# Optimization experiments

Hardware: AMD Instinct MI355X
Metric: run time of the kernel (lower is better)

The kernel has to match this reference:

```python
import jax, jax.numpy as jnp
import numpy as np

N_NODES = 40000
N_EDGES = 640000
N_GRAPHS = 64
D_IN = 128
HID = 200
OUT = 2


def _lin(key, fin, fout):
    # torch nn.Linear-style init: U(-1/sqrt(fin), 1/sqrt(fin))
    kw, kb = jax.random.split(key)
    s = 1.0 / np.sqrt(fin)
    W = jax.random.uniform(kw, (fin, fout), jnp.float32, -s, s)
    b = jax.random.uniform(kb, (fout,), jnp.float32, -s, s)
    return W, b


def setup_inputs() -> dict:
    key = jax.random.key(0)
    ks = jax.random.split(key, 10)
    x = jax.random.normal(ks[0], (N_NODES, D_IN), jnp.float32)
    edge_index = jax.random.randint(ks[1], (2, N_EDGES), 0, N_NODES, jnp.int32)
    batch = jnp.sort(jax.random.randint(ks[2], (N_NODES,), 0, N_GRAPHS, jnp.int32))
    W1, b1 = _lin(ks[3], D_IN, HID)
    W2, b2 = _lin(ks[4], HID, HID)
    W3, b3 = _lin(ks[5], HID, HID)
    Wg, bg = _lin(ks[6], HID, HID)
    Wc1, bc1 = _lin(ks[7], HID, HID // 2)
    Wc2, bc2 = _lin(ks[8], HID // 2, OUT)
    return {"x": x, "edge_index": edge_index, "batch": batch,
            "W1": W1, "b1": b1, "W2": W2, "b2": b2, "W3": W3, "b3": b3,
            "Wg": Wg, "bg": bg, "Wc1": Wc1, "bc1": bc1, "Wc2": Wc2, "bc2": bc2}


def reference(x, edge_index, batch, W1, b1, W2, b2, W3, b3, Wg, bg, Wc1, bc1, Wc2, bc2):
    n = x.shape[0]
    # GCNConv with self-loops + symmetric normalization (PyG defaults)
    loop = jnp.arange(n, dtype=edge_index.dtype)
    src = jnp.concatenate([edge_index[0], loop])  # [E+N]
    dst = jnp.concatenate([edge_index[1], loop])
    deg = jax.ops.segment_sum(jnp.ones(src.shape, x.dtype), dst, num_segments=n)
    dinv = jax.lax.rsqrt(jnp.maximum(deg, 1.0))  # deg >= 1 with self-loops
    norm = (dinv[src] * dinv[dst])[:, None]      # [E+N, 1]

    def gcn(h, W, b):
        m = (h @ W)[src] * norm                  # gather + scale per edge
        return jax.ops.segment_sum(m, dst, num_segments=n) + b

    h = jax.nn.relu(gcn(x, W1, b1))
    h = jax.nn.relu(gcn(h, W2, b2))
    h = jax.nn.relu(gcn(h, W3, b3))

    gate = jax.nn.sigmoid(h @ Wg + bg)
    hg = h * gate

    # global_mean_pool over batch assignment
    sums = jax.ops.segment_sum(hg, batch, num_segments=N_GRAPHS)
    cnt = jax.ops.segment_sum(jnp.ones((n,), x.dtype), batch, num_segments=N_GRAPHS)
    pooled = sums / jnp.maximum(cnt, 1.0)[:, None]

    # classifier (dropout is identity in eval)
    hidden = jax.nn.relu(pooled @ Wc1 + bc1)
    logits = hidden @ Wc2 + bc2                  # [N_GRAPHS, 2]
    return logits
```

## Files before the change

### kernel.cpp

```cpp
#include <hip/hip_runtime.h>

#define NG 64
#define HIDW 200
#define DIN 128
#define KPAD 224
#define POOL_NC 8

typedef _Float16 half4_t __attribute__((ext_vector_type(4)));
typedef _Float16 half8_t __attribute__((ext_vector_type(8)));
typedef float floatx4 __attribute__((ext_vector_type(4)));


__global__ void build_kernel(const int* __restrict__ dst, int* __restrict__ counts,
                             const int* __restrict__ batch, int* __restrict__ gs,
                             int E, int n) {
  int i = blockIdx.x * 256 + threadIdx.x;
  if (i < E) atomicAdd(&counts[dst[i]], 1);
  if (i < n) {
    int b = batch[i];
    if (i == 0) {
      for (int g = 0; g <= b; ++g) gs[g] = 0;
    } else {
      int bp = batch[i - 1];
      for (int g = bp + 1; g <= b; ++g) gs[g] = i;
    }
    if (i == n - 1) {
      for (int g = b + 1; g <= NG; ++g) gs[g] = n;
    }
  }
}


__global__ __launch_bounds__(256) void scan1_kernel(const int* __restrict__ counts,
                                                    int* __restrict__ blocksum,
                                                    float* __restrict__ dinv, int n) {
  __shared__ int s[256];
  int tid = threadIdx.x;
  int i = blockIdx.x * 256 + tid;
  int c = (i < n) ? counts[i] : 0;
  if (i < n) dinv[i] = rsqrtf((float)(c + 1));
  s[tid] = c;
  __syncthreads();
#pragma unroll
  for (int off = 128; off > 0; off >>= 1) {
    if (tid < off) s[tid] += s[tid + off];
    __syncthreads();
  }
  if (tid == 0) blocksum[blockIdx.x] = s[0];
}

__global__ __launch_bounds__(1024) void scan2_kernel(int* __restrict__ blocksum, int nb) {
  __shared__ int s[1024];
  int tid = threadIdx.x;
  int v = (tid < nb) ? blocksum[tid] : 0;
  s[tid] = v;
  __syncthreads();
  for (int off = 1; off < 1024; off <<= 1) {
    int t = (tid >= off) ? s[tid - off] : 0;
    __syncthreads();
    s[tid] += t;
    __syncthreads();
  }
  if (tid < nb) blocksum[tid] = s[tid] - v;
}

__global__ __launch_bounds__(256) void scan3_kernel(const int* __restrict__ counts,
                                                    const int* __restrict__ blocksum,
                                                    int* __restrict__ row_ptr, int n) {
  __shared__ int s[256];
  int tid = threadIdx.x;
  int i = blockIdx.x * 256 + tid;
  int c = (i < n) ? counts[i] : 0;
  s[tid] = c;
  __syncthreads();
  for (int off = 1; off < 256; off <<= 1) {
    int t = (tid >= off) ? s[tid - off] : 0;
    __syncthreads();
    s[tid] += t;
    __syncthreads();
  }
  int base = blocksum[blockIdx.x];
  if (i < n) row_ptr[i] = base + s[tid] - c;
  if (i == n - 1) row_ptr[n] = base + s[tid];
}

__global__ void fill_kernel(const int* __restrict__ src, const int* __restrict__ dst,
                            const int* __restrict__ row_ptr, int* __restrict__ fill,
                            int* __restrict__ csr_src, int E) {
  int e = blockIdx.x * 256 + threadIdx.x;
  if (e >= E) return;
  int d = dst[e];
  int pos = row_ptr[d] + atomicAdd(&fill[d], 1);
  csr_src[pos] = src[e];
}


__global__ void wprep_kernel(const float* __restrict__ W1, const float* __restrict__ W2,
                             const float* __restrict__ W3, const float* __restrict__ Wg,
                             _Float16* __restrict__ o1h, _Float16* __restrict__ o1l,
                             _Float16* __restrict__ o2h, _Float16* __restrict__ o2l,
                             _Float16* __restrict__ o3h, _Float16* __restrict__ o3l,
                             _Float16* __restrict__ ogh, _Float16* __restrict__ ogl) {
  int wsel = blockIdx.y;
  const float* W = (wsel == 0) ? W1 : (wsel == 1) ? W2 : (wsel == 2) ? W3 : Wg;
  _Float16* WTh = (wsel == 0) ? o1h : (wsel == 1) ? o2h : (wsel == 2) ? o3h : ogh;
  _Float16* WTl = (wsel == 0) ? o1l : (wsel == 1) ? o2l : (wsel == 2) ? o3l : ogl;
  int K  = (wsel == 0) ? DIN : HIDW;
  int KP = (wsel == 0) ? DIN : KPAD;
  int idx = blockIdx.x * 256 + threadIdx.x;
  if (idx >= 256 * KP) return;
  int col = idx / KP, k = idx % KP;
  float v = (col < HIDW && k < K) ? W[(long)k * HIDW + col] : 0.f;
  _Float16 h = (_Float16)v;
  WTh[idx] = h;
  WTl[idx] = (_Float16)(v - (float)h);
}


__global__ void cvt_kernel(const float* __restrict__ x, const float* __restrict__ dinv,
                           _Float16* __restrict__ g0, int n) {
  int t = blockIdx.x * 256 + threadIdx.x;
  if (t >= n * 32) return;
  int node = t >> 5, q = t & 31;
  float di = dinv[node];
  float4 v = *(const float4*)&x[(long)node * 128 + q * 4];
  half4_t r = {(_Float16)(di * v.x), (_Float16)(di * v.y),
               (_Float16)(di * v.z), (_Float16)(di * v.w)};
  ((half4_t*)g0)[(long)node * 32 + q] = r;
}


template <int C>
__global__ __launch_bounds__(256) void agg_kernel(const _Float16* __restrict__ g,
                                                  const int* __restrict__ row_ptr,
                                                  const int* __restrict__ csr_src,
                                                  const float* __restrict__ dinv,
                                                  _Float16* __restrict__ out, int n) {
  int node = blockIdx.x * 4 + (threadIdx.x >> 6);
  int lane = threadIdx.x & 63;
  if (node >= n || lane >= C) return;
  const half4_t* __restrict__ hp = (const half4_t*)g;
  int e0 = row_ptr[node], e1 = row_ptr[node + 1];
  half4_t self = hp[(long)node * C + lane];
  float ax = (float)self.x, ay = (float)self.y;
  float az = (float)self.z, aw = (float)self.w;

  int e = e0;
  for (; e + 16 <= e1; e += 16) {
    int sI[16];
#pragma unroll
    for (int j = 0; j < 16; ++j) sI[j] = csr_src[e + j];
    half4_t vv[16];
#pragma unroll
    for (int j = 0; j < 16; ++j) vv[j] = hp[(long)sI[j] * C + lane];
#pragma unroll
    for (int j = 0; j < 16; ++j) {
      ax += (float)vv[j].x; ay += (float)vv[j].y;
      az += (float)vv[j].z; aw += (float)vv[j].w;
    }
  }
  if (e + 8 <= e1) {
    int sI[8];
#pragma unroll
    for (int j = 0; j < 8; ++j) sI[j] = csr_src[e + j];
    half4_t vv[8];
#pragma unroll
    for (int j = 0; j < 8; ++j) vv[j] = hp[(long)sI[j] * C + lane];
#pragma unroll
    for (int j = 0; j < 8; ++j) {
      ax += (float)vv[j].x; ay += (float)vv[j].y;
      az += (float)vv[j].z; aw += (float)vv[j].w;
    }
    e += 8;
  }
  if (e + 4 <= e1) {
    int sI[4];
#pragma unroll
    for (int j = 0; j < 4; ++j) sI[j] = csr_src[e + j];
    half4_t vv[4];
#pragma unroll
    for (int j = 0; j < 4; ++j) vv[j] = hp[(long)sI[j] * C + lane];
#pragma unroll
    for (int j = 0; j < 4; ++j) {
      ax += (float)vv[j].x; ay += (float)vv[j].y;
      az += (float)vv[j].z; aw += (float)vv[j].w;
    }
    e += 4;
  }
  for (; e < e1; ++e) {
    int s = csr_src[e];
    half4_t v = hp[(long)s * C + lane];
    ax += (float)v.x; ay += (float)v.y; az += (float)v.z; aw += (float)v.w;
  }
  float di = dinv[node];
  half4_t r = {(_Float16)(di * ax), (_Float16)(di * ay),
               (_Float16)(di * az), (_Float16)(di * aw)};
  ((half4_t*)out)[(long)node * C + lane] = r;
}


template <int KP, int MODE, int DSCALE>
__global__ __launch_bounds__(256, 2) void mgemm_kernel(const _Float16* __restrict__ A,
                                                       const _Float16* __restrict__ WTh,
                                                       const _Float16* __restrict__ WTl,
                                                       const float* __restrict__ bias,
                                                       const float* __restrict__ dinv,
                                                       _Float16* __restrict__ out, int N) {
  constexpr int LDK = KP + 8;
  __shared__ _Float16 Bh[64][LDK];
  __shared__ _Float16 Bl[64][LDK];
  int tid = threadIdx.x;
  int strip = blockIdx.x & 3;
  int rg = blockIdx.x >> 2;
  int col0 = strip * 64;

  {
    int c = tid >> 2;
    int ks = (tid & 3) * (KP / 4);
    const _Float16* gh = WTh + (long)(col0 + c) * KP + ks;
    const _Float16* gl = WTl + (long)(col0 + c) * KP + ks;
#pragma unroll
    for (int j = 0; j < KP / 32; ++j) {
      *(half8_t*)&Bh[c][ks + j * 8] = *(const half8_t*)(gh + j * 8);
      *(half8_t*)&Bl[c][ks + j * 8] = *(const half8_t*)(gl + j * 8);
    }
  }
  __syncthreads();

  int lane = tid & 63;
  int wid = tid >> 6;
  int row0 = rg * 256 + wid * 64;
  if (row0 >= N) return;
  int l15 = lane & 15;
  int lq = lane >> 4;

  const _Float16* __restrict__ pa = A + (long)(row0 + l15) * KP + lq * 8;

  floatx4 acc[4][4];
#pragma unroll
  for (int i = 0; i < 4; ++i)
#pragma unroll
    for (int j = 0; j < 4; ++j) acc[i][j] = (floatx4){0.f, 0.f, 0.f, 0.f};

#pragma unroll
  for (int k0 = 0; k0 < KP; k0 += 32) {
    half8_t a[4];
#pragma unroll
    for (int rf = 0; rf < 4; ++rf)
      a[rf] = *(const half8_t*)(pa + (long)rf * 16 * KP + k0);
#pragma unroll
    for (int cf = 0; cf < 4; ++cf) {
      half8_t bh = *(const half8_t*)&Bh[cf * 16 + l15][k0 + lq * 8];
#pragma unroll
      for (int rf = 0; rf < 4; ++rf)
        acc[rf][cf] = __builtin_amdgcn_mfma_f32_16x16x32_f16(a[rf], bh, acc[rf][cf], 0, 0, 0);
    }
#pragma unroll
    for (int cf = 0; cf < 4; ++cf) {
      half8_t bl = *(const half8_t*)&Bl[cf * 16 + l15][k0 + lq * 8];
#pragma unroll
      for (int rf = 0; rf < 4; ++rf)
        acc[rf][cf] = __builtin_amdgcn_mfma_f32_16x16x32_f16(a[rf], bl, acc[rf][cf], 0, 0, 0);
    }
  }

#pragma unroll
  for (int cf = 0; cf < 4; ++cf) {
    int col = col0 + cf * 16 + l15;
    if (col >= KPAD) continue;
    float bs = (col < HIDW) ? bias[col] : 0.f;
#pragma unroll
    for (int rf = 0; rf < 4; ++rf) {
      int rbase = row0 + rf * 16 + lq * 4;
#pragma unroll
      for (int j = 0; j < 4; ++j) {
        int row = rbase + j;
        float v = acc[rf][cf][j] + bs;
        if (MODE == 1) v = fmaxf(v, 0.f);
        if (MODE == 2) {
          float hv = (float)A[(long)row * KP + col];
          v = hv * (1.f / (1.f + __expf(-v)));
        }
        if (DSCALE) v *= dinv[row];
        if (col >= HIDW) v = 0.f;
        out[(long)row * KPAD + col] = (_Float16)v;
      }
    }
  }
}


__global__ __launch_bounds__(256) void pool_partial_kernel(const _Float16* __restrict__ gated,
                                                           const int* __restrict__ gs,
                                                           float* __restrict__ partial, int n) {
  int g = blockIdx.x;
  int c = blockIdx.y;
  int f = threadIdx.x;
  int s = gs[g], e = gs[g + 1];
  int len = e - s;
  int chunk = (len + POOL_NC - 1) / POOL_NC;
  int i0 = s + c * chunk;
  int i1 = i0 + chunk; if (i1 > e) i1 = e;
  if (f < HIDW) {
    float acc = 0.f;
    for (int i = i0; i < i1; ++i) acc += (float)gated[(long)i * KPAD + f];
    partial[(g * POOL_NC + c) * HIDW + f] = acc;
  }
}


__global__ void classifier_kernel(const float* __restrict__ partial,
                                  const int* __restrict__ gs,
                                  const float* __restrict__ Wc1, const float* __restrict__ bc1,
                                  const float* __restrict__ Wc2, const float* __restrict__ bc2,
                                  float* __restrict__ out) {
  int g = blockIdx.x;
  int tid = threadIdx.x;
  __shared__ float pg[HIDW];
  __shared__ float hid[100];
  if (tid < HIDW) {
    float acc = 0.f;
#pragma unroll
    for (int c = 0; c < POOL_NC; ++c) acc += partial[(g * POOL_NC + c) * HIDW + tid];
    float cnt = fmaxf((float)(gs[g + 1] - gs[g]), 1.f);
    pg[tid] = acc / cnt;
  }
  __syncthreads();
  if (tid < 100) {
    float a = bc1[tid];
    for (int k = 0; k < HIDW; ++k) a = fmaf(pg[k], Wc1[k * 100 + tid], a);
    hid[tid] = fmaxf(a, 0.f);
  }
  __syncthreads();
  if (tid < 2) {
    float a = bc2[tid];
    for (int k = 0; k < 100; ++k) a = fmaf(hid[k], Wc2[k * 2 + tid], a);
    out[g * 2 + tid] = a;
  }
}


extern "C" void kernel_launch(void* const* d_in, const int* in_sizes, int n_in,
                              void* d_out, int out_size, void* d_ws, size_t ws_size,
                              hipStream_t stream) {
  const float* x    = (const float*)d_in[0];
  const int*   ei   = (const int*)d_in[1];
  const int*   batch= (const int*)d_in[2];
  const float* W1 = (const float*)d_in[3];  const float* b1 = (const float*)d_in[4];
  const float* W2 = (const float*)d_in[5];  const float* b2 = (const float*)d_in[6];
  const float* W3 = (const float*)d_in[7];  const float* b3 = (const float*)d_in[8];
  const float* Wg = (const float*)d_in[9];  const float* bg = (const float*)d_in[10];
  const float* Wc1= (const float*)d_in[11]; const float* bc1= (const float*)d_in[12];
  const float* Wc2= (const float*)d_in[13]; const float* bc2= (const float*)d_in[14];
  float* out = (float*)d_out;

  const int n = in_sizes[0] / DIN;
  const int E = in_sizes[1] / 2;
  const int* src = ei;
  const int* dst = ei + E;
  const int nb256 = (n + 255) / 256;

  int* counts   = (int*)d_ws;
  int* fill     = counts + n;
  int* row_ptr  = fill + n;
  int* gs       = row_ptr + (n + 4);
  int* blocksum = gs + 68;
  float* dinv   = (float*)(blocksum + 1024);
  int* csr_src  = (int*)(dinv + n);
  float* partial= (float*)(csr_src + E);
  _Float16* wt1h = (_Float16*)(partial + NG * POOL_NC * HIDW);
  _Float16* wt1l = wt1h + 256 * 128;
  _Float16* wt2h = wt1l + 256 * 128;
  _Float16* wt2l = wt2h + 256 * KPAD;
  _Float16* wt3h = wt2l + 256 * KPAD;
  _Float16* wt3l = wt3h + 256 * KPAD;
  _Float16* wtgh = wt3l + 256 * KPAD;
  _Float16* wtgl = wtgh + 256 * KPAD;
  _Float16* xh   = wtgl + 256 * KPAD;
  _Float16* bufA = xh + (long)n * DIN;
  _Float16* bufB = bufA + (long)n * KPAD;

  hipMemsetAsync(counts, 0, (size_t)2 * n * sizeof(int), stream);

  dim3 wgrid((256 * KPAD + 255) / 256, 4);
  wprep_kernel<<<wgrid, 256, 0, stream>>>(W1, W2, W3, Wg, wt1h, wt1l, wt2h, wt2l,
                                          wt3h, wt3l, wtgh, wtgl);

  int eb = (E + 255) / 256;
  build_kernel<<<eb, 256, 0, stream>>>(dst, counts, batch, gs, E, n);
  scan1_kernel<<<nb256, 256, 0, stream>>>(counts, blocksum, dinv, n);
  cvt_kernel<<<(n * 32 + 255) / 256, 256, 0, stream>>>(x, dinv, xh, n);
  scan2_kernel<<<1, 1024, 0, stream>>>(blocksum, nb256);
  scan3_kernel<<<nb256, 256, 0, stream>>>(counts, blocksum, row_ptr, n);
  fill_kernel<<<eb, 256, 0, stream>>>(src, dst, row_ptr, fill, csr_src, E);

  int ab = (n + 3) / 4;
  int gb = 4 * ((n + 255) / 256);

  agg_kernel<32><<<ab, 256, 0, stream>>>(xh, row_ptr, csr_src, dinv, bufA, n);
  mgemm_kernel<DIN, 1, 1><<<gb, 256, 0, stream>>>(bufA, wt1h, wt1l, b1, dinv, bufB, n);
  agg_kernel<56><<<ab, 256, 0, stream>>>(bufB, row_ptr, csr_src, dinv, bufA, n);
  mgemm_kernel<KPAD, 1, 1><<<gb, 256, 0, stream>>>(bufA, wt2h, wt2l, b2, dinv, bufB, n);
  agg_kernel<56><<<ab, 256, 0, stream>>>(bufB, row_ptr, csr_src, dinv, bufA, n);
  mgemm_kernel<KPAD, 1, 0><<<gb, 256, 0, stream>>>(bufA, wt3h, wt3l, b3, dinv, bufB, n);
  mgemm_kernel<KPAD, 2, 0><<<gb, 256, 0, stream>>>(bufB, wtgh, wtgl, bg, dinv, bufA, n);
  dim3 pgrid(NG, POOL_NC);
  pool_partial_kernel<<<pgrid, 256, 0, stream>>>(bufA, gs, partial, n);
  classifier_kernel<<<NG, 256, 0, stream>>>(partial, gs, Wc1, bc1, Wc2, bc2, out);
}
```

Before: 355.4 us.

## Slice feature layout into 32-column panels and degree-sort nodes for aggregation

Changes the activation layout from row-major [n][KPAD] to column-sliced panels of 32 halfs per node, so each aggregation block gathers 64-byte rows from one slice, which makes the gather working set per slice smaller and more cache-friendly. Nodes are bucketed by in-degree with a histogram counting sort, and aggregation walks them in that order so wavefront lanes see similar edge counts. The GEMM, gate and pooling kernels are updated to read and write the sliced layout, and aggregation stores use nontemporal hints. It adds atomics to the scan kernels and a permutation indirection per node, and shortens the gather unroll from 16 to 4.

```diff
diff --git a/kernel.cpp b/kernel.cpp
--- a/kernel.cpp
+++ b/kernel.cpp
@@ -33,12 +33,16 @@
 
 __global__ __launch_bounds__(256) void scan1_kernel(const int* __restrict__ counts,
                                                     int* __restrict__ blocksum,
-                                                    float* __restrict__ dinv, int n) {
+                                                    float* __restrict__ dinv,
+                                                    int* __restrict__ hist, int n) {
   __shared__ int s[256];
   int tid = threadIdx.x;
   int i = blockIdx.x * 256 + tid;
   int c = (i < n) ? counts[i] : 0;
-  if (i < n) dinv[i] = rsqrtf((float)(c + 1));
+  if (i < n) {
+    dinv[i] = rsqrtf((float)(c + 1));
+    atomicAdd(&hist[c < 63 ? c : 63], 1);
+  }
   s[tid] = c;
   __syncthreads();
 #pragma unroll
@@ -49,9 +53,16 @@
   if (tid == 0) blocksum[blockIdx.x] = s[0];
 }
 
-__global__ __launch_bounds__(1024) void scan2_kernel(int* __restrict__ blocksum, int nb) {
+
+__global__ __launch_bounds__(1024) void scan2_kernel(int* __restrict__ blocksum,
+                                                     int* __restrict__ hist, int nb) {
   __shared__ int s[1024];
   int tid = threadIdx.x;
+  if (tid == 0) {
+    int run = 0;
+#pragma unroll
+    for (int d = 0; d < 64; ++d) { int c = hist[d]; hist[d] = run; run += c; }
+  }
   int v = (tid < nb) ? blocksum[tid] : 0;
   s[tid] = v;
   __syncthreads();
@@ -64,9 +75,13 @@
   if (tid < nb) blocksum[tid] = s[tid] - v;
 }
 
+
 __global__ __launch_bounds__(256) void scan3_kernel(const int* __restrict__ counts,
                                                     const int* __restrict__ blocksum,
-                                                    int* __restrict__ row_ptr, int n) {
+                                                    int* __restrict__ row_ptr,
+                                                    const int* __restrict__ hist,
+                                                    int* __restrict__ histfill,
+                                                    int* __restrict__ perm, int n) {
   __shared__ int s[256];
   int tid = threadIdx.x;
   int i = blockIdx.x * 256 + tid;
@@ -80,7 +95,12 @@
     __syncthreads();
   }
   int base = blocksum[blockIdx.x];
-  if (i < n) row_ptr[i] = base + s[tid] - c;
+  if (i < n) {
+    row_ptr[i] = base + s[tid] - c;
+    int d = c < 63 ? c : 63;
+    int pos = hist[d] + atomicAdd(&histfill[d], 1);
+    perm[pos] = i;
+  }
   if (i == n - 1) row_ptr[n] = base + s[tid];
 }
 
@@ -126,76 +146,62 @@
   float4 v = *(const float4*)&x[(long)node * 128 + q * 4];
   half4_t r = {(_Float16)(di * v.x), (_Float16)(di * v.y),
                (_Float16)(di * v.z), (_Float16)(di * v.w)};
-  ((half4_t*)g0)[(long)node * 32 + q] = r;
-}
-
-
-template <int C>
+  ((half4_t*)g0)[((long)(q >> 3) * n + node) * 8 + (q & 7)] = r;
+}
+
+
+template <int NSLICE>
 __global__ __launch_bounds__(256) void agg_kernel(const _Float16* __restrict__ g,
                                                   const int* __restrict__ row_ptr,
                                                   const int* __restrict__ csr_src,
                                                   const float* __restrict__ dinv,
+                                                  const int* __restrict__ perm,
                                                   _Float16* __restrict__ out, int n) {
-  int node = blockIdx.x * 4 + (threadIdx.x >> 6);
+  int slot = blockIdx.x & 7;
+  int nb = blockIdx.x >> 3;
   int lane = threadIdx.x & 63;
-  if (node >= n || lane >= C) return;
-  const half4_t* __restrict__ hp = (const half4_t*)g;
+  int wv = threadIdx.x >> 6;
+  int q = lane & 7;
+  int nl = (wv << 3) + (lane >> 3);
+  int slice, idx;
+  if (NSLICE == 7) {
+    if (slot == 7) return;
+    slice = slot;
+    idx = nb * 32 + nl;
+  } else {
+    slice = slot >> 1;
+    idx = (nb * 2 + (slot & 1)) * 32 + nl;
+  }
+  if (idx >= n) return;
+  int node = perm[idx];
+  const half4_t* __restrict__ hp = (const half4_t*)g + (long)slice * n * 8;
   int e0 = row_ptr[node], e1 = row_ptr[node + 1];
-  half4_t self = hp[(long)node * C + lane];
+  half4_t self = hp[node * 8 + q];
   float ax = (float)self.x, ay = (float)self.y;
   float az = (float)self.z, aw = (float)self.w;
 
   int e = e0;
-  for (; e + 16 <= e1; e += 16) {
-    int sI[16];
-#pragma unroll
-    for (int j = 0; j < 16; ++j) sI[j] = csr_src[e + j];
-    half4_t vv[16];
-#pragma unroll
-    for (int j = 0; j < 16; ++j) vv[j] = hp[(long)sI[j] * C + lane];
-#pragma unroll
-    for (int j = 0; j < 16; ++j) {
-      ax += (float)vv[j].x; ay += (float)vv[j].y;
-      az += (float)vv[j].z; aw += (float)vv[j].w;
-    }
-  }
-  if (e + 8 <= e1) {
-    int sI[8];
-#pragma unroll
-    for (int j = 0; j < 8; ++j) sI[j] = csr_src[e + j];
-    half4_t vv[8];
-#pragma unroll
-    for (int j = 0; j < 8; ++j) vv[j] = hp[(long)sI[j] * C + lane];
-#pragma unroll
-    for (int j = 0; j < 8; ++j) {
-      ax += (float)vv[j].x; ay += (float)vv[j].y;
-      az += (float)vv[j].z; aw += (float)vv[j].w;
-    }
-    e += 8;
-  }
-  if (e + 4 <= e1) {
-    int sI[4];
-#pragma unroll
-    for (int j = 0; j < 4; ++j) sI[j] = csr_src[e + j];
-    half4_t vv[4];
-#pragma unroll
-    for (int j = 0; j < 4; ++j) vv[j] = hp[(long)sI[j] * C + lane];
-#pragma unroll
-    for (int j = 0; j < 4; ++j) {
-      ax += (float)vv[j].x; ay += (float)vv[j].y;
-      az += (float)vv[j].z; aw += (float)vv[j].w;
-    }
-    e += 4;
+  for (; e + 4 <= e1; e += 4) {
+    int s0 = csr_src[e + 0], s1 = csr_src[e + 1];
+    int s2 = csr_src[e + 2], s3 = csr_src[e + 3];
+    half4_t v0 = hp[s0 * 8 + q];
+    half4_t v1 = hp[s1 * 8 + q];
+    half4_t v2 = hp[s2 * 8 + q];
+    half4_t v3 = hp[s3 * 8 + q];
+    ax += (float)v0.x + (float)v1.x + (float)v2.x + (float)v3.x;
+    ay += (float)v0.y + (float)v1.y + (float)v2.y + (float)v3.y;
+    az += (float)v0.z + (float)v1.z + (float)v2.z + (float)v3.z;
+    aw += (float)v0.w + (float)v1.w + (float)v2.w + (float)v3.w;
   }
   for (; e < e1; ++e) {
     int s = csr_src[e];
-    half4_t v = hp[(long)s * C + lane];
+    half4_t v = hp[s * 8 + q];
     ax += (float)v.x; ay += (float)v.y; az += (float)v.z; aw += (float)v.w;
   }
   float di = dinv[node];
   half4_t r = {(_Float16)(di * ax), (_Float16)(di * ay),
                (_Float16)(di * az), (_Float16)(di * aw)};
-  ((half4_t*)out)[(long)node * C + lane] = r;
+  __builtin_nontemporal_store(r, (half4_t*)out + (long)slice * n * 8 + node * 8 + q);
 }
 
 
@@ -234,8 +240,6 @@
   int l15 = lane & 15;
   int lq = lane >> 4;
 
-  const _Float16* __restrict__ pa = A + (long)(row0 + l15) * KP + lq * 8;
-
   floatx4 acc[4][4];
 #pragma unroll
   for (int i = 0; i < 4; ++i)
@@ -244,10 +248,11 @@
 
 #pragma unroll
   for (int k0 = 0; k0 < KP; k0 += 32) {
+    const _Float16* as = A + ((long)(k0 >> 5) * N + row0 + l15) * 32 + lq * 8;
     half8_t a[4];
 #pragma unroll
     for (int rf = 0; rf < 4; ++rf)
-      a[rf] = *(const half8_t*)(pa + (long)rf * 16 * KP + k0);
+      a[rf] = *(const half8_t*)(as + rf * 16 * 32);
 #pragma unroll
     for (int cf = 0; cf < 4; ++cf) {
       half8_t bh = *(const half8_t*)&Bh[cf * 16 + l15][k0 + lq * 8];
@@ -269,6 +274,7 @@
     int col = col0 + cf * 16 + l15;
     if (col >= KPAD) continue;
     float bs = (col < HIDW) ? bias[col] : 0.f;
+    long obase = ((long)(col >> 5) * N) * 32 + (col & 31);
 #pragma unroll
     for (int rf = 0; rf < 4; ++rf) {
       int rbase = row0 + rf * 16 + lq * 4;
@@ -278,12 +284,12 @@
         float v = acc[rf][cf][j] + bs;
         if (MODE == 1) v = fmaxf(v, 0.f);
         if (MODE == 2) {
-          float hv = (float)A[(long)row * KP + col];
+          float hv = (float)A[((long)(col >> 5) * N + row) * 32 + (col & 31)];
           v = hv * (1.f / (1.f + __expf(-v)));
         }
         if (DSCALE) v *= dinv[row];
         if (col >= HIDW) v = 0.f;
-        out[(long)row * KPAD + col] = (_Float16)v;
+        out[obase + (long)row * 32] = (_Float16)v;
       }
     }
   }
@@ -302,8 +308,9 @@
   int i0 = s + c * chunk;
   int i1 = i0 + chunk; if (i1 > e) i1 = e;
   if (f < HIDW) {
+    const _Float16* p = gated + ((long)(f >> 5) * n) * 32 + (f & 31);
     float acc = 0.f;
-    for (int i = i0; i < i1; ++i) acc += (float)gated[(long)i * KPAD + f];
+    for (int i = i0; i < i1; ++i) acc += (float)p[(long)i * 32];
     partial[(g * POOL_NC + c) * HIDW + f] = acc;
   }
 }
@@ -362,10 +369,13 @@
 
   int* counts   = (int*)d_ws;
   int* fill     = counts + n;
-  int* row_ptr  = fill + n;
+  int* hist     = fill + n;
+  int* histfill = hist + 64;
+  int* row_ptr  = histfill + 64;
   int* gs       = row_ptr + (n + 4);
   int* blocksum = gs + 68;
-  float* dinv   = (float*)(blocksum + 1024);
+  int* perm     = blocksum + 1024;
+  float* dinv   = (float*)(perm + n);
   int* csr_src  = (int*)(dinv + n);
   float* partial= (float*)(csr_src + E);
   _Float16* wt1h = (_Float16*)(partial + NG * POOL_NC * HIDW);
@@ -380,7 +390,7 @@
   _Float16* bufA = xh + (long)n * DIN;
   _Float16* bufB = bufA + (long)n * KPAD;
 
-  hipMemsetAsync(counts, 0, (size_t)2 * n * sizeof(int), stream);
+  hipMemsetAsync(counts, 0, ((size_t)2 * n + 128) * sizeof(int), stream);
 
   dim3 wgrid((256 * KPAD + 255) / 256, 4);
   wprep_kernel<<<wgrid, 256, 0, stream>>>(W1, W2, W3, Wg, wt1h, wt1l, wt2h, wt2l,
@@ -388,20 +398,21 @@
 
   int eb = (E + 255) / 256;
   build_kernel<<<eb, 256, 0, stream>>>(dst, counts, batch, gs, E, n);
-  scan1_kernel<<<nb256, 256, 0, stream>>>(counts, blocksum, dinv, n);
+  scan1_kernel<<<nb256, 256, 0, stream>>>(counts, blocksum, dinv, hist, n);
   cvt_kernel<<<(n * 32 + 255) / 256, 256, 0, stream>>>(x, dinv, xh, n);
-  scan2_kernel<<<1, 1024, 0, stream>>>(blocksum, nb256);
-  scan3_kernel<<<nb256, 256, 0, stream>>>(counts, blocksum, row_ptr, n);
+  scan2_kernel<<<1, 1024, 0, stream>>>(blocksum, hist, nb256);
+  scan3_kernel<<<nb256, 256, 0, stream>>>(counts, blocksum, row_ptr, hist, histfill, perm, n);
   fill_kernel<<<eb, 256, 0, stream>>>(src, dst, row_ptr, fill, csr_src, E);
 
-  int ab = (n + 3) / 4;
+  int ag7 = 8 * ((n + 31) / 32);
+  int ag4 = 8 * ((n + 63) / 64);
   int gb = 4 * ((n + 255) / 256);
 
-  agg_kernel<32><<<ab, 256, 0, stream>>>(xh, row_ptr, csr_src, dinv, bufA, n);
+  agg_kernel<4><<<ag4, 256, 0, stream>>>(xh, row_ptr, csr_src, dinv, perm, bufA, n);
   mgemm_kernel<DIN, 1, 1><<<gb, 256, 0, stream>>>(bufA, wt1h, wt1l, b1, dinv, bufB, n);
-  agg_kernel<56><<<ab, 256, 0, stream>>>(bufB, row_ptr, csr_src, dinv, bufA, n);
+  agg_kernel<7><<<ag7, 256, 0, stream>>>(bufB, row_ptr, csr_src, dinv, perm, bufA, n);
   mgemm_kernel<KPAD, 1, 1><<<gb, 256, 0, stream>>>(bufA, wt2h, wt2l, b2, dinv, bufB, n);
-  agg_kernel<56><<<ab, 256, 0, stream>>>(bufB, row_ptr, csr_src, dinv, bufA, n);
+  agg_kernel<7><<<ag7, 256, 0, stream>>>(bufB, row_ptr, csr_src, dinv, perm, bufA, n);
   mgemm_kernel<KPAD, 1, 0><<<gb, 256, 0, stream>>>(bufA, wt3h, wt3l, b3, dinv, bufB, n);
   mgemm_kernel<KPAD, 2, 0><<<gb, 256, 0, stream>>>(bufB, wtgh, wtgl, bg, dinv, bufA, n);
   dim3 pgrid(NG, POOL_NC);
```

New measurement: 554.0 us. +55.9%, slower.
